# Kernel optimization log

Measured on AMD Instinct MI355X. Metric: run time of the kernel, lower is better.

The kernel has to match this reference:

```python
import jax, jax.numpy as jnp
import numpy as np

B, D, K = 2048, 512, 32  # pairs, input_dim, feature_map_dim


def setup_inputs() -> dict:
    key = jax.random.key(0)
    k1, k2, kw, kv, ku = jax.random.split(key, 5)
    x1 = jax.random.normal(k1, (B, D), dtype=jnp.float32)
    x2 = jax.random.normal(k2, (B, D), dtype=jnp.float32)
    # glorot-style scaled params
    W = jax.random.normal(kw, (D, D, K), dtype=jnp.float32) * (1.0 / np.sqrt(D))
    V = jax.random.normal(kv, (K, 2 * D), dtype=jnp.float32) * (1.0 / np.sqrt(2 * D))
    U = jax.random.normal(ku, (K, 1), dtype=jnp.float32)
    b = jnp.zeros((K,), dtype=jnp.float32)
    return {"x1": x1, "x2": x2, "W": W, "V": V, "U": U, "b": b}


def reference(x1, x2, W, V, U, b):
    # Bilinear term: h[b,k] = x1[b]^T W[:,:,k] x2[b]
    h = jnp.einsum('bd,dek,be->bk', x1, W, x2)
    # Linear term: V[k] . concat(x1, x2)   (loop's V_out, batched)
    v_out = jnp.concatenate([x1, x2], axis=1) @ V.T  # [B, K]
    scores = jax.nn.relu(h + v_out + b)              # inneract
    # output per pair: sum_k U[k] * scores[k]
    return scores @ U[:, 0]  # [B]
```

## Files before the change

### kernel.cpp

```cpp
#include <hip/hip_runtime.h>
#include <hip/hip_bf16.h>


#define BATCH 2048
#define DIM 512
#define KF 32
#define NCOL (DIM * KF)
#define JT (NCOL / 128)

typedef __attribute__((ext_vector_type(8))) short bf16x8;
typedef __attribute__((ext_vector_type(4))) float f32x4;
typedef __attribute__((address_space(1))) const unsigned int gas_u32;
typedef __attribute__((address_space(3))) unsigned int las_u32;

static __device__ __forceinline__ ushort f2bf(float x) {
    __hip_bfloat16 h = __float2bfloat16(x);
    union { __hip_bfloat16 h; ushort u; } cv; cv.h = h;
    return cv.u;
}

__global__ void cvt_x1_kernel(const float4* __restrict__ x, ushort4* __restrict__ o) {
    int i = blockIdx.x * 256 + threadIdx.x;
    float4 v = x[i];
    ushort4 r;
    r.x = f2bf(v.x); r.y = f2bf(v.y); r.z = f2bf(v.z); r.w = f2bf(v.w);
    o[i] = r;
}

__global__ void cvt_wt_kernel(const float* __restrict__ W, ushort* __restrict__ Wt) {
    __shared__ ushort lt[64][65];
    const int n0 = blockIdx.x * 64;
    const int d0 = blockIdx.y * 64;
    const int t = threadIdx.x;
    #pragma unroll
    for (int it = 0; it < 4; ++it) {
        int q = it * 256 + t;
        int dl = q >> 4;
        int n4 = (q & 15) * 4;
        float4 v = *(const float4*)&W[(size_t)(d0 + dl) * NCOL + n0 + n4];
        lt[n4 + 0][dl] = f2bf(v.x);
        lt[n4 + 1][dl] = f2bf(v.y);
        lt[n4 + 2][dl] = f2bf(v.z);
        lt[n4 + 3][dl] = f2bf(v.w);
    }
    __syncthreads();
    #pragma unroll
    for (int it = 0; it < 4; ++it) {
        int q = it * 256 + t;
        int nl = q >> 4;
        int d4 = (q & 15) * 4;
        ushort4 o;
        o.x = lt[nl][d4 + 0]; o.y = lt[nl][d4 + 1];
        o.z = lt[nl][d4 + 2]; o.w = lt[nl][d4 + 3];
        *(ushort4*)&Wt[(size_t)(n0 + nl) * DIM + d0 + d4] = o;
    }
}

__global__ void vout_kernel(const float* __restrict__ x1,
                            const float* __restrict__ x2,
                            const float* __restrict__ V,
                            float* __restrict__ vout) {
    __shared__ float xs[8][1024];
    const int b0 = blockIdx.x * 8;
    const int t = threadIdx.x;
    #pragma unroll
    for (int it = 0; it < 4; ++it) {
        int q = it * 256 + t;
        int r = q >> 7;
        int c = (q & 127) * 4;
        *(float4*)&xs[r][c]       = *(const float4*)&x1[(size_t)(b0 + r) * DIM + c];
        *(float4*)&xs[r][512 + c] = *(const float4*)&x2[(size_t)(b0 + r) * DIM + c];
    }
    __syncthreads();
    const int lane = t & 63, w = t >> 6;
    #pragma unroll
    for (int rr = 0; rr < 2; ++rr) {
        const int r = w * 2 + rr;
        for (int k = 0; k < KF; ++k) {
            const float* vrow = V + (size_t)k * 1024;
            float s = 0.0f;
            #pragma unroll
            for (int i = 0; i < 4; ++i) {
                float4 vv = *(const float4*)&vrow[i * 256 + lane * 4];
                float4 xv = *(const float4*)&xs[r][i * 256 + lane * 4];
                s += vv.x * xv.x + vv.y * xv.y + vv.z * xv.z + vv.w * xv.w;
            }
            #pragma unroll
            for (int off = 32; off; off >>= 1) s += __shfl_down(s, off);
            if (lane == 0) vout[(size_t)(b0 + r) * KF + k] = s;
        }
    }
}

__global__ void gemm_fused_kernel(const ushort* __restrict__ Ab,
                                  const ushort* __restrict__ Bt,
                                  const float* __restrict__ x2,
                                  float* __restrict__ hpart) {
    __shared__ __align__(16) char smem[16384];
    ushort* As = (ushort*)smem;
    ushort* Bs = (ushort*)(smem + 8192);
    float*  hp = (float*)smem;

    const int j = blockIdx.x;
    const int i = blockIdx.y;
    const int t = threadIdx.x;
    const int lane = t & 63, wid = t >> 6;
    const int wr = wid >> 1, wc = wid & 1;
    const int row0 = i * 128, col0 = j * 128;
    const int l15 = lane & 15, lk = (lane >> 4) * 8, lh = lane >> 4;

    const int sidx0 = t * 8;
    const int sr0 = sidx0 >> 5, sc0_ = sidx0 & 31;
    const int sidx1 = 2048 + t * 8;
    const int sr1 = sidx1 >> 5, sc1_ = sidx1 & 31;

    f32x4 acc[4][4] = {};

    for (int kt = 0; kt < DIM; kt += 32) {
        __builtin_amdgcn_global_load_lds(
            (gas_u32*)&Ab[(size_t)(row0 + sr0) * DIM + kt + sc0_],
            (las_u32*)&As[sidx0], 16, 0, 0);
        __builtin_amdgcn_global_load_lds(
            (gas_u32*)&Ab[(size_t)(row0 + sr1) * DIM + kt + sc1_],
            (las_u32*)&As[sidx1], 16, 0, 0);
        __builtin_amdgcn_global_load_lds(
            (gas_u32*)&Bt[(size_t)(col0 + sr0) * DIM + kt + sc0_],
            (las_u32*)&Bs[sidx0], 16, 0, 0);
        __builtin_amdgcn_global_load_lds(
            (gas_u32*)&Bt[(size_t)(col0 + sr1) * DIM + kt + sc1_],
            (las_u32*)&Bs[sidx1], 16, 0, 0);
        __syncthreads();
        bf16x8 af[4], bfr[4];
        #pragma unroll
        for (int m = 0; m < 4; ++m)
            af[m] = *(bf16x8*)&As[(wr * 64 + m * 16 + l15) * 32 + lk];
        #pragma unroll
        for (int n = 0; n < 4; ++n)
            bfr[n] = *(bf16x8*)&Bs[(wc * 64 + n * 16 + l15) * 32 + lk];
        #pragma unroll
        for (int m = 0; m < 4; ++m)
            #pragma unroll
            for (int n = 0; n < 4; ++n)
                acc[m][n] = __builtin_amdgcn_mfma_f32_16x16x32_bf16(af[m], bfr[n], acc[m][n], 0, 0, 0);
        __syncthreads();
    }

    const int e0 = j * 4 + wc * 2;
    if (wc == 0) {
        #pragma unroll
        for (int m = 0; m < 4; ++m) {
            #pragma unroll
            for (int reg = 0; reg < 4; ++reg) {
                int row = wr * 64 + m * 16 + lh * 4 + reg;
                float xa = x2[(size_t)(row0 + row) * DIM + e0];
                float xb = x2[(size_t)(row0 + row) * DIM + e0 + 1];
                hp[row * 32 + l15]      = acc[m][0][reg] * xa + acc[m][2][reg] * xb;
                hp[row * 32 + 16 + l15] = acc[m][1][reg] * xa + acc[m][3][reg] * xb;
            }
        }
    }
    __syncthreads();
    if (wc == 1) {
        #pragma unroll
        for (int m = 0; m < 4; ++m) {
            #pragma unroll
            for (int reg = 0; reg < 4; ++reg) {
                int row = wr * 64 + m * 16 + lh * 4 + reg;
                float xa = x2[(size_t)(row0 + row) * DIM + e0];
                float xb = x2[(size_t)(row0 + row) * DIM + e0 + 1];
                hp[row * 32 + l15]      += acc[m][0][reg] * xa + acc[m][2][reg] * xb;
                hp[row * 32 + 16 + l15] += acc[m][1][reg] * xa + acc[m][3][reg] * xb;
            }
        }
    }
    __syncthreads();
    #pragma unroll
    for (int q = 0; q < 4; ++q) {
        int idx = q * 1024 + t * 4;
        int row = idx >> 5, kf = idx & 31;
        *(float4*)&hpart[(size_t)(row0 + row) * (JT * KF) + j * KF + kf] = *(float4*)&hp[idx];
    }
}

__global__ void reduce_out_kernel(const float* __restrict__ hpart,
                                  const float* __restrict__ vout,
                                  const float* __restrict__ U,
                                  const float* __restrict__ bias,
                                  float* __restrict__ out) {
    const int b = blockIdx.x;
    const int t = threadIdx.x;
    __shared__ float4 hsm[256];
    __shared__ float hk[32];

    const float* hb = hpart + (size_t)b * (JT * KF);
    float4 a4 = {0.f, 0.f, 0.f, 0.f};
    #pragma unroll
    for (int p = 0; p < 4; ++p) {
        float4 v = *(const float4*)&hb[p * 1024 + t * 4];
        a4.x += v.x; a4.y += v.y; a4.z += v.z; a4.w += v.w;
    }
    hsm[t] = a4;
    __syncthreads();
    if (t < 8) {
        float4 s = {0.f, 0.f, 0.f, 0.f};
        #pragma unroll
        for (int g = 0; g < 32; ++g) {
            float4 v = hsm[g * 8 + t];
            s.x += v.x; s.y += v.y; s.z += v.z; s.w += v.w;
        }
        hk[t * 4 + 0] = s.x; hk[t * 4 + 1] = s.y;
        hk[t * 4 + 2] = s.z; hk[t * 4 + 3] = s.w;
    }
    __syncthreads();

    float val = 0.0f;
    if (t < 32) {
        float sc = hk[t] + vout[(size_t)b * KF + t] + bias[t];
        sc = fmaxf(sc, 0.0f);
        val = sc * U[t];
    }
    if (t < 64) {
        #pragma unroll
        for (int off = 16; off; off >>= 1) val += __shfl_down(val, off);
        if (t == 0) out[b] = val;
    }
}

extern "C" void kernel_launch(void* const* d_in, const int* in_sizes, int n_in,
                              void* d_out, int out_size, void* d_ws, size_t ws_size,
                              hipStream_t stream) {
    const float* x1   = (const float*)d_in[0];
    const float* x2   = (const float*)d_in[1];
    const float* W    = (const float*)d_in[2];
    const float* V    = (const float*)d_in[3];
    const float* U    = (const float*)d_in[4];
    const float* bias = (const float*)d_in[5];
    float* out = (float*)d_out;

    char* ws = (char*)d_ws;
    ushort* x1b = (ushort*)ws;
    ushort* Wt  = (ushort*)(ws + (size_t)2 * 1024 * 1024);
    float*  hp  = (float*)(ws + (size_t)18 * 1024 * 1024);
    float*  vo  = (float*)(ws + (size_t)50 * 1024 * 1024);

    cvt_x1_kernel<<<dim3(1024), dim3(256), 0, stream>>>((const float4*)x1, (ushort4*)x1b);
    cvt_wt_kernel<<<dim3(256, 8), dim3(256), 0, stream>>>(W, Wt);
    vout_kernel<<<dim3(BATCH / 8), dim3(256), 0, stream>>>(x1, x2, V, vo);
    gemm_fused_kernel<<<dim3(JT, 16), dim3(256), 0, stream>>>(x1b, Wt, x2, hp);
    reduce_out_kernel<<<dim3(BATCH), dim3(256), 0, stream>>>(hp, vo, U, bias, out);
}
```

Measured before the change: 175.0 us.

## Fuse prep kernels into one launch and swizzle GEMM LDS tiles

```diff
diff --git a/kernel.cpp b/kernel.cpp
--- a/kernel.cpp
+++ b/kernel.cpp
@@ -19,75 +19,90 @@
     return cv.u;
 }
 
-__global__ void cvt_x1_kernel(const float4* __restrict__ x, ushort4* __restrict__ o) {
-    int i = blockIdx.x * 256 + threadIdx.x;
-    float4 v = x[i];
-    ushort4 r;
-    r.x = f2bf(v.x); r.y = f2bf(v.y); r.z = f2bf(v.z); r.w = f2bf(v.w);
-    o[i] = r;
-}
-
-__global__ void cvt_wt_kernel(const float* __restrict__ W, ushort* __restrict__ Wt) {
-    __shared__ ushort lt[64][65];
-    const int n0 = blockIdx.x * 64;
-    const int d0 = blockIdx.y * 64;
+__global__ void fused_prep_kernel(const float* __restrict__ x1,
+                                  const float* __restrict__ x2,
+                                  const float* __restrict__ W,
+                                  const float* __restrict__ V,
+                                  ushort* __restrict__ x1b,
+                                  ushort* __restrict__ Wt,
+                                  float* __restrict__ vout) {
+    __shared__ __align__(16) char sbuf[32768];
+    const int bx = blockIdx.x;
     const int t = threadIdx.x;
-    #pragma unroll
-    for (int it = 0; it < 4; ++it) {
-        int q = it * 256 + t;
-        int dl = q >> 4;
-        int n4 = (q & 15) * 4;
-        float4 v = *(const float4*)&W[(size_t)(d0 + dl) * NCOL + n0 + n4];
-        lt[n4 + 0][dl] = f2bf(v.x);
-        lt[n4 + 1][dl] = f2bf(v.y);
-        lt[n4 + 2][dl] = f2bf(v.z);
-        lt[n4 + 3][dl] = f2bf(v.w);
-    }
-    __syncthreads();
-    #pragma unroll
-    for (int it = 0; it < 4; ++it) {
-        int q = it * 256 + t;
-        int nl = q >> 4;
-        int d4 = (q & 15) * 4;
-        ushort4 o;
-        o.x = lt[nl][d4 + 0]; o.y = lt[nl][d4 + 1];
-        o.z = lt[nl][d4 + 2]; o.w = lt[nl][d4 + 3];
-        *(ushort4*)&Wt[(size_t)(n0 + nl) * DIM + d0 + d4] = o;
-    }
-}
-
-__global__ void vout_kernel(const float* __restrict__ x1,
-                            const float* __restrict__ x2,
-                            const float* __restrict__ V,
-                            float* __restrict__ vout) {
-    __shared__ float xs[8][1024];
-    const int b0 = blockIdx.x * 8;
-    const int t = threadIdx.x;
-    #pragma unroll
-    for (int it = 0; it < 4; ++it) {
-        int q = it * 256 + t;
-        int r = q >> 7;
-        int c = (q & 127) * 4;
-        *(float4*)&xs[r][c]       = *(const float4*)&x1[(size_t)(b0 + r) * DIM + c];
-        *(float4*)&xs[r][512 + c] = *(const float4*)&x2[(size_t)(b0 + r) * DIM + c];
-    }
-    __syncthreads();
-    const int lane = t & 63, w = t >> 6;
-    #pragma unroll
-    for (int rr = 0; rr < 2; ++rr) {
-        const int r = w * 2 + rr;
-        for (int k = 0; k < KF; ++k) {
-            const float* vrow = V + (size_t)k * 1024;
-            float s = 0.0f;
-            #pragma unroll
-            for (int i = 0; i < 4; ++i) {
-                float4 vv = *(const float4*)&vrow[i * 256 + lane * 4];
-                float4 xv = *(const float4*)&xs[r][i * 256 + lane * 4];
-                s += vv.x * xv.x + vv.y * xv.y + vv.z * xv.z + vv.w * xv.w;
+
+    if (bx < 256) {
+        float (*xs)[1024] = (float(*)[1024])sbuf;
+        const int b0 = bx * 8;
+        #pragma unroll
+        for (int it = 0; it < 4; ++it) {
+            int q = it * 256 + t;
+            int r = q >> 7;
+            int c = (q & 127) * 4;
+            *(float4*)&xs[r][c]       = *(const float4*)&x1[(size_t)(b0 + r) * DIM + c];
+            *(float4*)&xs[r][512 + c] = *(const float4*)&x2[(size_t)(b0 + r) * DIM + c];
+        }
+        __syncthreads();
+        const int lane = t & 63, w = t >> 6;
+        #pragma unroll
+        for (int rr = 0; rr < 2; ++rr) {
+            const int r = w * 2 + rr;
+            float4 xv[4];
+            #pragma unroll
+            for (int i = 0; i < 4; ++i)
+                xv[i] = *(const float4*)&xs[r][i * 256 + lane * 4];
+            #pragma unroll
+            for (int k0 = 0; k0 < KF; k0 += 4) {
+                float s[4] = {0.f, 0.f, 0.f, 0.f};
+                #pragma unroll
+                for (int kk = 0; kk < 4; ++kk) {
+                    const float* vrow = V + (size_t)(k0 + kk) * 1024;
+                    #pragma unroll
+                    for (int i = 0; i < 4; ++i) {
+                        float4 vv = *(const float4*)&vrow[i * 256 + lane * 4];
+                        s[kk] += vv.x * xv[i].x + vv.y * xv[i].y + vv.z * xv[i].z + vv.w * xv[i].w;
+                    }
+                }
+                #pragma unroll
+                for (int kk = 0; kk < 4; ++kk) {
+                    float v = s[kk];
+                    #pragma unroll
+                    for (int off = 32; off; off >>= 1) v += __shfl_down(v, off);
+                    if (lane == 0) vout[(size_t)(b0 + r) * KF + k0 + kk] = v;
+                }
             }
-            #pragma unroll
-            for (int off = 32; off; off >>= 1) s += __shfl_down(s, off);
-            if (lane == 0) vout[(size_t)(b0 + r) * KF + k] = s;
+        }
+    } else if (bx < 1280) {
+        int i = (bx - 256) * 256 + t;
+        float4 v = *((const float4*)x1 + i);
+        ushort4 r;
+        r.x = f2bf(v.x); r.y = f2bf(v.y); r.z = f2bf(v.z); r.w = f2bf(v.w);
+        *((ushort4*)x1b + i) = r;
+    } else {
+        ushort (*lt)[65] = (ushort(*)[65])sbuf;
+        const int bxl = bx - 1280;
+        const int n0 = (bxl >> 3) * 64;
+        const int d0 = (bxl & 7) * 64;
+        #pragma unroll
+        for (int it = 0; it < 4; ++it) {
+            int q = it * 256 + t;
+            int dl = q >> 4;
+            int n4 = (q & 15) * 4;
+            float4 v = *(const float4*)&W[(size_t)(d0 + dl) * NCOL + n0 + n4];
+            lt[n4 + 0][dl] = f2bf(v.x);
+            lt[n4 + 1][dl] = f2bf(v.y);
+            lt[n4 + 2][dl] = f2bf(v.z);
+            lt[n4 + 3][dl] = f2bf(v.w);
+        }
+        __syncthreads();
+        #pragma unroll
+        for (int it = 0; it < 4; ++it) {
+            int q = it * 256 + t;
+            int nl = q >> 4;
+            int d4 = (q & 15) * 4;
+            ushort4 o;
+            o.x = lt[nl][d4 + 0]; o.y = lt[nl][d4 + 1];
+            o.z = lt[nl][d4 + 2]; o.w = lt[nl][d4 + 3];
+            *(ushort4*)&Wt[(size_t)(n0 + nl) * DIM + d0 + d4] = o;
         }
     }
 }
@@ -109,34 +124,33 @@
     const int row0 = i * 128, col0 = j * 128;
     const int l15 = lane & 15, lk = (lane >> 4) * 8, lh = lane >> 4;
 
-    const int sidx0 = t * 8;
-    const int sr0 = sidx0 >> 5, sc0_ = sidx0 & 31;
-    const int sidx1 = 2048 + t * 8;
-    const int sr1 = sidx1 >> 5, sc1_ = sidx1 & 31;
+    const int sr = t >> 2;
+    const int scsw = ((t & 3) ^ ((sr & 6) >> 1)) * 8;
+    const int lksw = lk ^ ((l15 & 6) << 2);
 
     f32x4 acc[4][4] = {};
 
     for (int kt = 0; kt < DIM; kt += 32) {
         __builtin_amdgcn_global_load_lds(
-            (gas_u32*)&Ab[(size_t)(row0 + sr0) * DIM + kt + sc0_],
-            (las_u32*)&As[sidx0], 16, 0, 0);
-        __builtin_amdgcn_global_load_lds(
-            (gas_u32*)&Ab[(size_t)(row0 + sr1) * DIM + kt + sc1_],
-            (las_u32*)&As[sidx1], 16, 0, 0);
-        __builtin_amdgcn_global_load_lds(
-            (gas_u32*)&Bt[(size_t)(col0 + sr0) * DIM + kt + sc0_],
-            (las_u32*)&Bs[sidx0], 16, 0, 0);
-        __builtin_amdgcn_global_load_lds(
-            (gas_u32*)&Bt[(size_t)(col0 + sr1) * DIM + kt + sc1_],
-            (las_u32*)&Bs[sidx1], 16, 0, 0);
+            (gas_u32*)&Ab[(size_t)(row0 + sr) * DIM + kt + scsw],
+            (las_u32*)&As[t * 8], 16, 0, 0);
+        __builtin_amdgcn_global_load_lds(
+            (gas_u32*)&Ab[(size_t)(row0 + 64 + sr) * DIM + kt + scsw],
+            (las_u32*)&As[2048 + t * 8], 16, 0, 0);
+        __builtin_amdgcn_global_load_lds(
+            (gas_u32*)&Bt[(size_t)(col0 + sr) * DIM + kt + scsw],
+            (las_u32*)&Bs[t * 8], 16, 0, 0);
+        __builtin_amdgcn_global_load_lds(
+            (gas_u32*)&Bt[(size_t)(col0 + 64 + sr) * DIM + kt + scsw],
+            (las_u32*)&Bs[2048 + t * 8], 16, 0, 0);
         __syncthreads();
         bf16x8 af[4], bfr[4];
         #pragma unroll
         for (int m = 0; m < 4; ++m)
-            af[m] = *(bf16x8*)&As[(wr * 64 + m * 16 + l15) * 32 + lk];
+            af[m] = *(bf16x8*)&As[(wr * 64 + m * 16 + l15) * 32 + lksw];
         #pragma unroll
         for (int n = 0; n < 4; ++n)
-            bfr[n] = *(bf16x8*)&Bs[(wc * 64 + n * 16 + l15) * 32 + lk];
+            bfr[n] = *(bf16x8*)&Bs[(wc * 64 + n * 16 + l15) * 32 + lksw];
         #pragma unroll
         for (int m = 0; m < 4; ++m)
             #pragma unroll
@@ -243,9 +257,7 @@
     float*  hp  = (float*)(ws + (size_t)18 * 1024 * 1024);
     float*  vo  = (float*)(ws + (size_t)50 * 1024 * 1024);
 
-    cvt_x1_kernel<<<dim3(1024), dim3(256), 0, stream>>>((const float4*)x1, (ushort4*)x1b);
-    cvt_wt_kernel<<<dim3(256, 8), dim3(256), 0, stream>>>(W, Wt);
-    vout_kernel<<<dim3(BATCH / 8), dim3(256), 0, stream>>>(x1, x2, V, vo);
+    fused_prep_kernel<<<dim3(3328), dim3(256), 0, stream>>>(x1, x2, W, V, x1b, Wt, vo);
     gemm_fused_kernel<<<dim3(JT, 16), dim3(256), 0, stream>>>(x1b, Wt, x2, hp);
     reduce_out_kernel<<<dim3(BATCH), dim3(256), 0, stream>>>(hp, vo, U, bias, out);
 }
```

Measured after the change: 155.6 us. -11.0%, faster.
